# Optimization experiments

Measured on AMD Instinct MI355X. Metric: run time of the kernel, lower is better.

Reference implementation:

```python
import jax, jax.numpy as jnp
import numpy as np

N_NODES, N_EDGES, B, L = 20000, 320000, 64, 48
EMB, OUT, HEADS, HID = 256, 64, 4, 512
S_DIM, R_DIM = 64, 64
TIME_NUM, CAT_NUM = 48, 201


def lrelu(x, s=0.2):
    return jnp.where(x >= 0, x, s * x)


def gru_cell(x, h, Wi, Wh, bi, bh):
    # PyTorch GRUCell math
    gi = x @ Wi.T + bi
    gh = h @ Wh.T + bh
    ir, iz, ig = jnp.split(gi, 3, axis=-1)
    hr, hz, hg = jnp.split(gh, 3, axis=-1)
    r = jax.nn.sigmoid(ir + hr)
    z = jax.nn.sigmoid(iz + hz)
    n = jnp.tanh(ig + r * hg)
    return (1.0 - z) * n + z * h


def gru_seq(x, Wi, Wh, bi, bh, reverse=False):
    # x: [B,L,D] -> [B,L,H]
    xs = jnp.swapaxes(x, 0, 1)
    if reverse:
        xs = xs[::-1]
    h0 = jnp.zeros((x.shape[0], Wh.shape[1]), x.dtype)

    def step(h, xt):
        h2 = gru_cell(xt, h, Wi, Wh, bi, bh)
        return h2, h2

    _, ys = jax.lax.scan(step, h0, xs)
    if reverse:
        ys = ys[::-1]
    return jnp.swapaxes(ys, 0, 1)


def setup_inputs() -> dict:
    key = jax.random.key(0)
    ks = iter(jax.random.split(key, 64))
    f32 = jnp.float32

    def rn(shape, s=0.1):
        return (s * jax.random.normal(next(ks), shape)).astype(f32)

    inp = {
        'graph_x': jnp.arange(N_NODES),
        'edge_index': jax.random.randint(next(ks), (2, N_EDGES), 0, N_NODES),
        'edge_attr': jax.random.uniform(next(ks), (N_EDGES,), f32),
        'batch_x': jax.random.randint(next(ks), (B, L), 0, N_NODES),
        'batch_time': jax.random.randint(next(ks), (B, L), 0, TIME_NUM),
        'batch_cat': jax.random.randint(next(ks), (B, L), 0, CAT_NUM),
        'poi_time': jax.random.randint(next(ks), (N_NODES,), 0, TIME_NUM),
        'poi_cat': jax.random.randint(next(ks), (N_NODES,), 0, CAT_NUM),
        # params
        'node_emb': rn((N_NODES, EMB), 1.0),
        'W_gat': rn((EMB, HEADS * OUT), 0.05),
        'att_src': rn((HEADS, OUT), 0.05),
        'att_dst': rn((HEADS, OUT), 0.05),
        'gat_bias': rn((HEADS * OUT,)),
        'time_table': rn((TIME_NUM, EMB), 1.0),
        'cat_table': rn((CAT_NUM, EMB), 1.0),
        'W_w': rn((EMB, 3 * EMB)), 'b_w': rn((EMB,)),
        'Wi_f': rn((3 * HID, EMB), 0.05), 'Wh_f': rn((3 * HID, HID), 0.05),
        'bi_f': jnp.zeros((3 * HID,), f32), 'bh_f': jnp.zeros((3 * HID,), f32),
        'Wi_bw': rn((3 * HID, EMB), 0.05), 'Wh_bw': rn((3 * HID, HID), 0.05),
        'bi_bw': jnp.zeros((3 * HID,), f32), 'bh_bw': jnp.zeros((3 * HID,), f32),
        'Wi_u': rn((3 * HID, 2 * HID), 0.05), 'Wh_u': rn((3 * HID, HID), 0.05),
        'bi_u': jnp.zeros((3 * HID,), f32), 'bh_u': jnp.zeros((3 * HID,), f32),
        'Ws_m': rn((S_DIM, 2 * HID)), 'bs_m': rn((S_DIM,)),
        'Ws_lv': rn((S_DIM, 2 * HID)), 'bs_lv': rn((S_DIM,)),
        'Wr_m': rn((R_DIM, HID)), 'br_m': rn((R_DIM,)),
        'Wr_lv': rn((R_DIM, HID)), 'br_lv': rn((R_DIM,)),
        'Wp1_i': rn((3 * HID, R_DIM), 0.05), 'Wp1_h': rn((3 * HID, HID), 0.05),
        'bp1_i': jnp.zeros((3 * HID,), f32), 'bp1_h': jnp.zeros((3 * HID,), f32),
        'Wp2_i': rn((3 * HID, HID), 0.05), 'Wp2_h': rn((3 * HID, HID), 0.05),
        'bp2_i': jnp.zeros((3 * HID,), f32), 'bp2_h': jnp.zeros((3 * HID,), f32),
        'Wpm': rn((R_DIM, HID)), 'bpm': rn((R_DIM,)),
        'Wplv': rn((R_DIM, HID)), 'bplv': rn((R_DIM,)),
        'Wd': rn((N_NODES, S_DIM + R_DIM)), 'bd': rn((N_NODES,)),
    }
    return inp


def forward(graph_x, edge_index, edge_attr, batch_x, batch_time, batch_cat,
            poi_time, poi_cat, node_emb, W_gat, att_src, att_dst, gat_bias,
            time_table, cat_table, W_w, b_w, Wi_f, Wh_f, bi_f, bh_f,
            Wi_bw, Wh_bw, bi_bw, bh_bw, Wi_u, Wh_u, bi_u, bh_u,
            Ws_m, bs_m, Ws_lv, bs_lv, Wr_m, br_m, Wr_lv, br_lv,
            Wp1_i, Wp1_h, bp1_i, bp1_h, Wp2_i, Wp2_h, bp2_i, bp2_h,
            Wpm, bpm, Wplv, bplv, Wd, bd):
    Bn, Ln = batch_x.shape
    N = node_emb.shape[0]
    heads, C = att_src.shape

    # --- weighted GAT layer over the POI graph ---
    h = node_emb[graph_x]                                   # [N, EMB]
    xW = (h @ W_gat).reshape(N, heads, C)                   # [N, H, C]
    src, dst = edge_index[0], edge_index[1]
    e = lrelu((xW * att_src).sum(-1)[src] + (xW * att_dst).sum(-1)[dst])  # [E, H]
    emax = jax.ops.segment_max(e, dst, num_segments=N)
    a = jnp.exp(e - emax[dst])
    asum = jax.ops.segment_sum(a, dst, num_segments=N)
    att = a / (asum[dst] + 1e-16)
    msg = (att * edge_attr[:, None])[:, :, None] * xW[src]  # [E, H, C]
    p = jax.ops.segment_sum(msg, dst, num_segments=N).reshape(N, heads * C) + gat_bias

    # --- per-step feature build ---
    p_h = p[batch_x]                                        # [B, L, EMB]
    t_e = time_table[batch_time]
    c_e = cat_table[batch_cat]
    ph = jnp.concatenate([p_h, t_e, c_e], axis=2) @ W_w.T + b_w  # [B, L, EMB]

    # --- posterior encode: biGRU -> s, uniGRU -> r ---
    f_fwd = gru_seq(ph, Wi_f, Wh_f, bi_f, bh_f)
    f_bwd = gru_seq(ph, Wi_bw, Wh_bw, bi_bw, bh_bw, reverse=True)
    features = jnp.concatenate([f_fwd, f_bwd], axis=2)      # [B, L, 2H]
    Hh = Wh_f.shape[1]
    frontal = features[:, Ln - 1, :Hh]
    backward = features[:, 0, Hh:2 * Hh]
    g = jnp.concatenate([frontal, backward], axis=1)
    s_mean = lrelu(g @ Ws_m.T + bs_m)
    s_logvar = lrelu(g @ Ws_lv.T + bs_lv)

    key = jax.random.key(42)
    k1, k2, k3 = jax.random.split(key, 3)
    s_post = s_mean + jax.random.normal(k1, s_mean.shape, s_mean.dtype) * jnp.exp(0.5 * s_logvar)

    r_feat = gru_seq(features, Wi_u, Wh_u, bi_u, bh_u)      # [B, L, H]
    r_mean = r_feat @ Wr_m.T + br_m
    r_logvar = r_feat @ Wr_lv.T + br_lv
    r_post = r_mean + jax.random.normal(k2, r_mean.shape, r_mean.dtype) * jnp.exp(0.5 * r_logvar)

    # --- prior: 2-layer GRUCell unroll fed with shifted r_post ---
    Rd = r_post.shape[2]
    r_in = jnp.concatenate([jnp.zeros((Bn, 1, Rd), r_post.dtype), r_post[:, :-1]], axis=1)
    r_in_t = jnp.swapaxes(r_in, 0, 1)                       # [L, B, R]
    eps = jax.random.normal(k3, (Ln, Bn, Rd), r_post.dtype)

    def pstep(carry, xe):
        h1, h2 = carry
        rt, ep = xe
        h1 = gru_cell(rt, h1, Wp1_i, Wp1_h, bp1_i, bp1_h)
        h2 = gru_cell(h1, h2, Wp2_i, Wp2_h, bp2_i, bp2_h)
        mt = h2 @ Wpm.T + bpm
        lvt = h2 @ Wplv.T + bplv
        rp = mt + ep * jnp.exp(0.5 * lvt)
        return (h1, h2), (mt, lvt, rp)

    h10 = jnp.zeros((Bn, Hh), r_post.dtype)
    h20 = jnp.zeros((Bn, Hh), r_post.dtype)
    _, (ms, lvs, rps) = jax.lax.scan(pstep, (h10, h20), (r_in_t, eps))
    r_mean_prior = jnp.swapaxes(ms, 0, 1)
    r_logvar_prior = jnp.swapaxes(lvs, 0, 1)
    r_prior = jnp.swapaxes(rps, 0, 1)

    # --- decode ---
    s_expand = jnp.broadcast_to(s_post[:, None, :], (Bn, Ln, s_post.shape[1]))
    zf = jnp.concatenate([r_post, s_expand], axis=2)
    recon_x = zf @ Wd.T + bd                                # [B, L, node_num]
    return (s_mean, s_logvar, s_post, r_mean, r_logvar, r_post,
            r_mean_prior, r_logvar_prior, r_prior, recon_x)


def reference(graph_x, edge_index, edge_attr, batch_x, batch_time, batch_cat,
              poi_time, poi_cat, node_emb, W_gat, att_src, att_dst, gat_bias,
              time_table, cat_table, W_w, b_w, Wi_f, Wh_f, bi_f, bh_f,
              Wi_bw, Wh_bw, bi_bw, bh_bw, Wi_u, Wh_u, bi_u, bh_u,
              Ws_m, bs_m, Ws_lv, bs_lv, Wr_m, br_m, Wr_lv, br_lv,
              Wp1_i, Wp1_h, bp1_i, bp1_h, Wp2_i, Wp2_h, bp2_i, bp2_h,
              Wpm, bpm, Wplv, bplv, Wd, bd):
    return forward(graph_x, edge_index, edge_attr, batch_x, batch_time, batch_cat,
                   poi_time, poi_cat, node_emb, W_gat, att_src, att_dst, gat_bias,
                   time_table, cat_table, W_w, b_w, Wi_f, Wh_f, bi_f, bh_f,
                   Wi_bw, Wh_bw, bi_bw, bh_bw, Wi_u, Wh_u, bi_u, bh_u,
                   Ws_m, bs_m, Ws_lv, bs_lv, Wr_m, br_m, Wr_lv, br_lv,
                   Wp1_i, Wp1_h, bp1_i, bp1_h, Wp2_i, Wp2_h, bp2_i, bp2_h,
                   Wpm, bpm, Wplv, bplv, Wd, bd)
```

## Files before the change

kernel.cpp:

```cpp
#include <hip/hip_runtime.h>
#include <stdint.h>
#include <stddef.h>

#define DEV __device__ __forceinline__

typedef float f32x4 __attribute__((ext_vector_type(4)));
typedef short bf16x8 __attribute__((ext_vector_type(8)));

__host__ __device__ inline void tf2x32(uint32_t k0, uint32_t k1,
                                       uint32_t x0, uint32_t x1,
                                       uint32_t* o0, uint32_t* o1) {
  uint32_t ks2 = k0 ^ k1 ^ 0x1BD11BDAu;
  uint32_t ks[3] = {k0, k1, ks2};
  x0 += k0; x1 += k1;
  const uint32_t R[8] = {13u,15u,26u,6u,17u,29u,16u,24u};
  for (int r = 0; r < 5; ++r) {
    const uint32_t* rot = (r & 1) ? (R + 4) : R;
    for (int i = 0; i < 4; ++i) {
      x0 += x1;
      uint32_t d = rot[i];
      x1 = (x1 << d) | (x1 >> (32u - d));
      x1 ^= x0;
    }
    x0 += ks[(r + 1) % 3];
    x1 += ks[(r + 2) % 3] + (uint32_t)(r + 1);
  }
  *o0 = x0; *o1 = x1;
}

DEV float erfinv_approx(float x) {
  float w = -logf((1.0f - x) * (1.0f + x));
  float p;
  if (w < 5.0f) {
    w = w - 2.5f;
    p = 2.81022636e-08f;
    p = fmaf(p, w, 3.43273939e-07f);
    p = fmaf(p, w, -3.5233877e-06f);
    p = fmaf(p, w, -4.39150654e-06f);
    p = fmaf(p, w, 0.00021858087f);
    p = fmaf(p, w, -0.00125372503f);
    p = fmaf(p, w, -0.00417768164f);
    p = fmaf(p, w, 0.246640727f);
    p = fmaf(p, w, 1.50140941f);
  } else {
    w = sqrtf(w) - 3.0f;
    p = -0.000200214257f;
    p = fmaf(p, w, 0.000100950558f);
    p = fmaf(p, w, 0.00134934322f);
    p = fmaf(p, w, -0.00367342844f);
    p = fmaf(p, w, 0.00573950773f);
    p = fmaf(p, w, -0.0076224613f);
    p = fmaf(p, w, 0.00943887047f);
    p = fmaf(p, w, 1.00167406f);
    p = fmaf(p, w, 2.83297682f);
  }
  return p * x;
}

DEV float normal_part(uint32_t ka, uint32_t kb, uint32_t idx) {
  uint32_t b1, b2;
  tf2x32(ka, kb, 0u, idx, &b1, &b2);
  uint32_t bits = b1 ^ b2;
  float f = __uint_as_float((bits >> 9) | 0x3f800000u) - 1.0f;
  const float lo = -0.99999994f;
  float u = f * 2.0f + lo;
  u = fmaxf(lo, u);
  return 1.41421356f * erfinv_approx(u);
}

DEV float lrelu(float x) { return x >= 0.f ? x : 0.2f * x; }
DEV float sigm(float x) { return 1.0f / (1.0f + expf(-x)); }

DEV float gru_out(float ir, float iz, float ig, float hr, float hz, float hg, float hprev) {
  float r = sigm(ir + hr);
  float z = sigm(iz + hz);
  float n = tanhf(ig + r * hg);
  return (1.0f - z) * n + z * hprev;
}

DEV float dot4f(float4 a, float4 b, float acc) {
  return fmaf(a.x, b.x, fmaf(a.y, b.y, fmaf(a.z, b.z, fmaf(a.w, b.w, acc))));
}

template <int K4>
DEV void dot2(const float* __restrict__ h, const float* __restrict__ w0,
              const float* __restrict__ w1, float& a0, float& a1) {
  const float4* h4 = (const float4*)h;
  const float4* p0 = (const float4*)w0;
  const float4* p1 = (const float4*)w1;
  #pragma unroll 4
  for (int k = 0; k < K4; ++k) {
    float4 hv = h4[k];
    float4 v0 = p0[k], v1 = p1[k];
    a0 = dot4f(hv, v0, a0);
    a1 = dot4f(hv, v1, a1);
  }
}

template <int K4>
DEV void dotT3p(const float* __restrict__ hp, int b,
                const float* __restrict__ w0, const float* __restrict__ w1,
                const float* __restrict__ w2, float& a0, float& a1, float& a2) {
  const float4* __restrict__ w04 = (const float4*)w0;
  const float4* __restrict__ w14 = (const float4*)w1;
  const float4* __restrict__ w24 = (const float4*)w2;
  const float4* __restrict__ h4 = (const float4*)hp;
  #pragma unroll
  for (int k4 = 0; k4 < K4; ++k4) {
    float4 hv = h4[k4 * 64 + b];
    a0 = dot4f(w04[k4], hv, a0);
    a1 = dot4f(w14[k4], hv, a1);
    a2 = dot4f(w24[k4], hv, a2);
  }
}

template <int K4>
DEV void dotT3_lds(const float* __restrict__ hl, int b,
                   const float* __restrict__ w0, const float* __restrict__ w1,
                   const float* __restrict__ w2, float& a0, float& a1, float& a2) {
  const float4* __restrict__ h4 = (const float4*)hl;
  const float4* __restrict__ w04 = (const float4*)w0;
  const float4* __restrict__ w14 = (const float4*)w1;
  const float4* __restrict__ w24 = (const float4*)w2;
  #pragma unroll 8
  for (int k4 = 0; k4 < K4; ++k4) {
    float4 hv = h4[k4 * 64 + b];
    a0 = dot4f(w04[k4], hv, a0);
    a1 = dot4f(w14[k4], hv, a1);
    a2 = dot4f(w24[k4], hv, a2);
  }
}

template <int N16>
DEV void stage_lds(float* __restrict__ dst, const float* __restrict__ src) {
  const float4* __restrict__ s4 = (const float4*)src;
  float4* __restrict__ d4 = (float4*)dst;
  int tid = threadIdx.x;
  constexpr int CH = (N16 < 16) ? N16 : 16;
  #pragma unroll
  for (int r = 0; r < N16; r += CH) {
    float4 v[CH];
    #pragma unroll
    for (int u = 0; u < CH; ++u) v[u] = s4[(size_t)(r + u) * 256 + tid];
    #pragma unroll
    for (int u = 0; u < CH; ++u) d4[(size_t)(r + u) * 256 + tid] = v[u];
  }
}

DEV size_t pk(int k, int b) { return (size_t)(k >> 2) * 256 + b * 4 + (k & 3); }

DEV void coh_store_i(int* p, int v) {
  asm volatile("global_store_dword %0, %1, off sc0 sc1" :: "v"(p), "v"(v) : "memory");
}
DEV void coh_store_f(float* p, float v) {
  asm volatile("global_store_dword %0, %1, off sc0 sc1" :: "v"(p), "v"(v) : "memory");
}
DEV void coh_store_f4(float* p, f32x4 v) {
  asm volatile("global_store_dwordx4 %0, %1, off sc0 sc1" :: "v"(p), "v"(v) : "memory");
}
DEV int coh_load_i(const int* p) {
  int v;
  asm volatile("global_load_dword %0, %1, off sc0 sc1\n\ts_waitcnt vmcnt(0)"
               : "=v"(v) : "v"(p) : "memory");
  return v;
}

#define FSTRIDE 32

DEV void flag_barrier(int* __restrict__ flags, int nblk, int myidx, int gen) {
  asm volatile("s_waitcnt vmcnt(0)" ::: "memory");
  __syncthreads();
  if (threadIdx.x == 0) coh_store_i(flags + (size_t)myidx * FSTRIDE, gen);
  if ((int)threadIdx.x < nblk) {
    int spins = 0;
    while (coh_load_i(flags + (size_t)threadIdx.x * FSTRIDE) < gen) {
      __builtin_amdgcn_s_sleep(4);
      if (++spins > (1 << 21)) break;
    }
  }
  __syncthreads();
}

DEV void wait_group(const int* __restrict__ flags, int nblk, int thr) {
  if ((int)threadIdx.x < nblk) {
    int spins = 0;
    while (coh_load_i(flags + (size_t)threadIdx.x * FSTRIDE) < thr) {
      __builtin_amdgcn_s_sleep(4);
      if (++spins > (1 << 21)) break;
    }
  }
  __syncthreads();
}

DEV void store_packed_tile4(float* dst_t, const float (*smem)[64], int j0) {
  if (threadIdx.x < 64) {
    int bb = threadIdx.x;
    f32x4 v;
    v.x = smem[0][bb];
    v.y = smem[1][bb];
    v.z = smem[2][bb];
    v.w = smem[3][bb];
    coh_store_f4(dst_t + (size_t)(j0 >> 2) * 256 + bb * 4, v);
  }
}

#define GBM 128
#define GBN 128
#define GBK 16

__global__ __launch_bounds__(256) void gemm_nt(
    const float* __restrict__ A, const float* __restrict__ Bt,
    const float* __restrict__ bias, float* __restrict__ C,
    int M, int N, int K, const int* __restrict__ gatherA, int trGI) {
  __shared__ float As[GBK][GBM + 4];
  __shared__ float Bs[GBK][GBN + 4];
  const int bm = blockIdx.y * GBM;
  const int bn = blockIdx.x * GBN;
  const int tid = threadIdx.x;
  const int tx = tid & 15;
  const int ty = tid >> 4;
  float acc[8][8];
  #pragma unroll
  for (int i = 0; i < 8; ++i)
    #pragma unroll
    for (int j = 0; j < 8; ++j) acc[i][j] = 0.f;

  for (int k0 = 0; k0 < K; k0 += GBK) {
    #pragma unroll
    for (int s = 0; s < 2; ++s) {
      int f = tid + s * 256;
      int r = f >> 2, kq = f & 3;
      int row = bm + r;
      float4 v = make_float4(0.f, 0.f, 0.f, 0.f);
      if (row < M) {
        int ar = gatherA ? gatherA[row] : row;
        v = *(const float4*)&A[(size_t)ar * K + k0 + kq * 4];
      }
      As[kq * 4 + 0][r] = v.x;
      As[kq * 4 + 1][r] = v.y;
      As[kq * 4 + 2][r] = v.z;
      As[kq * 4 + 3][r] = v.w;
    }
    #pragma unroll
    for (int s = 0; s < 2; ++s) {
      int f = tid + s * 256;
      int r = f >> 2, kq = f & 3;
      int col = bn + r;
      float4 v = make_float4(0.f, 0.f, 0.f, 0.f);
      if (col < N) v = *(const float4*)&Bt[(size_t)col * K + k0 + kq * 4];
      Bs[kq * 4 + 0][r] = v.x;
      Bs[kq * 4 + 1][r] = v.y;
      Bs[kq * 4 + 2][r] = v.z;
      Bs[kq * 4 + 3][r] = v.w;
    }
    __syncthreads();
    #pragma unroll
    for (int kk = 0; kk < GBK; ++kk) {
      float4 a0 = *(const float4*)&As[kk][ty * 4];
      float4 a1 = *(const float4*)&As[kk][64 + ty * 4];
      float4 b0 = *(const float4*)&Bs[kk][tx * 4];
      float4 b1 = *(const float4*)&Bs[kk][64 + tx * 4];
      float av[8] = {a0.x, a0.y, a0.z, a0.w, a1.x, a1.y, a1.z, a1.w};
      float bv[8] = {b0.x, b0.y, b0.z, b0.w, b1.x, b1.y, b1.z, b1.w};
      #pragma unroll
      for (int i = 0; i < 8; ++i)
        #pragma unroll
        for (int j = 0; j < 8; ++j)
          acc[i][j] = fmaf(av[i], bv[j], acc[i][j]);
    }
    __syncthreads();
  }
  #pragma unroll
  for (int i = 0; i < 8; ++i) {
    int row = bm + ((i < 4) ? (ty * 4 + i) : (64 + ty * 4 + i - 4));
    if (row >= M) continue;
    if (trGI) {
      #pragma unroll
      for (int j = 0; j < 8; ++j) {
        int col = bn + ((j < 4) ? (tx * 4 + j) : (64 + tx * 4 + j - 4));
        if (col >= N) continue;
        float v = acc[i][j] + (bias ? bias[col] : 0.f);
        int bb = row / 48, tt = row - bb * 48;
        C[((size_t)tt * N + col) * 64 + bb] = v;
      }
    } else {
      #pragma unroll
      for (int g = 0; g < 2; ++g) {
        int col0 = bn + g * 64 + tx * 4;
        if (col0 + 3 >= N) continue;
        float4 v;
        v.x = acc[i][g * 4 + 0] + (bias ? bias[col0 + 0] : 0.f);
        v.y = acc[i][g * 4 + 1] + (bias ? bias[col0 + 1] : 0.f);
        v.z = acc[i][g * 4 + 2] + (bias ? bias[col0 + 2] : 0.f);
        v.w = acc[i][g * 4 + 3] + (bias ? bias[col0 + 3] : 0.f);
        *(float4*)&C[(size_t)row * N + col0] = v;
      }
    }
  }
}

__global__ void k_f32_to_bf16(const float* __restrict__ src,
                              unsigned short* __restrict__ dst, int n) {
  int i = blockIdx.x * 256 + threadIdx.x;
  if (i >= n) return;
  uint32_t u = __float_as_uint(src[i]);
  uint32_t r = (u + 0x7fffu + ((u >> 16) & 1u)) >> 16;
  dst[i] = (unsigned short)r;
}

__global__ __launch_bounds__(256) void gemm_bf16_mfma(
    const unsigned short* __restrict__ A16, const unsigned short* __restrict__ B16,
    const float* __restrict__ bias, float* __restrict__ C,
    int M, int N, int K) {
  int bm = blockIdx.x * 128;
  int bn = blockIdx.y * 128;
  int wave = threadIdx.x >> 6;
  int lane = threadIdx.x & 63;
  int wm = (wave & 1) * 64;
  int wn = (wave >> 1) * 64;
  int l15 = lane & 15;
  int kg = lane >> 4;
  f32x4 acc[4][4];
  #pragma unroll
  for (int mi = 0; mi < 4; ++mi)
    #pragma unroll
    for (int ni = 0; ni < 4; ++ni)
      acc[mi][ni] = (f32x4){0.f, 0.f, 0.f, 0.f};

  for (int kk = 0; kk < K; kk += 32) {
    bf16x8 afrag[4], bfrag[4];
    #pragma unroll
    for (int mi = 0; mi < 4; ++mi) {
      int row = bm + wm + mi * 16 + l15;
      afrag[mi] = *(const bf16x8*)&A16[(size_t)row * K + kk + kg * 8];
    }
    #pragma unroll
    for (int ni = 0; ni < 4; ++ni) {
      int col = bn + wn + ni * 16 + l15;
      if (col >= N) col = N - 1;
      bfrag[ni] = *(const bf16x8*)&B16[(size_t)col * K + kk + kg * 8];
    }
    #pragma unroll
    for (int mi = 0; mi < 4; ++mi)
      #pragma unroll
      for (int ni = 0; ni < 4; ++ni)
        acc[mi][ni] = __builtin_amdgcn_mfma_f32_16x16x32_bf16(
            afrag[mi], bfrag[ni], acc[mi][ni], 0, 0, 0);
  }
  #pragma unroll
  for (int mi = 0; mi < 4; ++mi) {
    #pragma unroll
    for (int ni = 0; ni < 4; ++ni) {
      int col = bn + wn + ni * 16 + l15;
      if (col >= N) continue;
      int rowb = bm + wm + mi * 16 + kg * 4;
      float bv = bias[col];
      #pragma unroll
      for (int r = 0; r < 4; ++r)
        C[(size_t)(rowb + r) * N + col] = acc[mi][ni][r] + bv;
    }
  }
}

__global__ void k_transpose(const float* __restrict__ W, float* __restrict__ Wt,
                            int rows, int cols) {
  int idx = blockIdx.x * 256 + threadIdx.x;
  if (idx >= rows * cols) return;
  int r = idx / cols, c = idx % cols;
  Wt[(size_t)c * rows + r] = W[idx];
}

__global__ void k_count_deg(const int* __restrict__ dst, int* __restrict__ deg, int nE) {
  int e = blockIdx.x * 256 + threadIdx.x;
  if (e < nE) atomicAdd(&deg[dst[e]], 1);
}

__global__ __launch_bounds__(1024) void k_scan(const int* __restrict__ deg,
                                               int* __restrict__ off,
                                               int* __restrict__ cursor, int n) {
  __shared__ int tmp[1024];
  __shared__ int carry_s;
  if (threadIdx.x == 0) carry_s = 0;
  __syncthreads();
  for (int base = 0; base < n; base += 1024) {
    int i = base + (int)threadIdx.x;
    int v = (i < n) ? deg[i] : 0;
    tmp[threadIdx.x] = v;
    __syncthreads();
    for (int s = 1; s < 1024; s <<= 1) {
      int t = (threadIdx.x >= (unsigned)s) ? tmp[threadIdx.x - s] : 0;
      __syncthreads();
      tmp[threadIdx.x] += t;
      __syncthreads();
    }
    int incl = tmp[threadIdx.x];
    int base_c = carry_s;
    int excl = incl - v;
    if (i < n) { off[i] = base_c + excl; cursor[i] = base_c + excl; }
    __syncthreads();
    if (threadIdx.x == 1023) carry_s = base_c + incl;
    __syncthreads();
  }
  if (threadIdx.x == 0) off[n] = carry_s;
}

__global__ void k_scatter(const int* __restrict__ dst, int* __restrict__ cursor,
                          int* __restrict__ csr, int nE) {
  int e = blockIdx.x * 256 + threadIdx.x;
  if (e < nE) {
    int pos = atomicAdd(&cursor[dst[e]], 1);
    csr[pos] = e;
  }
}

__global__ void k_alpha(const float* __restrict__ xW, const float* __restrict__ att_src,
                        const float* __restrict__ att_dst, float* __restrict__ as_,
                        float* __restrict__ ad_) {
  int i = blockIdx.x * 256 + threadIdx.x;
  if (i >= 80000) return;
  int n = i >> 2, h = i & 3;
  const float* xr = xW + (size_t)n * 256 + h * 64;
  const float* s = att_src + h * 64;
  const float* d = att_dst + h * 64;
  float a = 0.f, b = 0.f;
  dot2<16>(xr, s, d, a, b);
  as_[i] = a;
  ad_[i] = b;
}

__global__ __launch_bounds__(256) void k_gat_node(
    const float* __restrict__ xW, const float* __restrict__ as_,
    const float* __restrict__ ad_, const int* __restrict__ off,
    const int* __restrict__ csr, const int* __restrict__ esrc,
    const float* __restrict__ eattr, const float* __restrict__ gat_bias,
    float* __restrict__ p) {
  int n = blockIdx.x;
  int h = threadIdx.x >> 6;
  int c = threadIdx.x & 63;
  int s0 = off[n], s1 = off[n + 1];
  float adn = ad_[n * 4 + h];
  float m = -3.0e38f;
  for (int idx = s0; idx < s1; ++idx) {
    int e = csr[idx];
    int s = esrc[e];
    float ev = lrelu(as_[s * 4 + h] + adn);
    m = fmaxf(m, ev);
  }
  float sum = 0.f;
  for (int idx = s0; idx < s1; ++idx) {
    int e = csr[idx];
    int s = esrc[e];
    float ev = lrelu(as_[s * 4 + h] + adn);
    sum += expf(ev - m);
  }
  float acc = 0.f;
  for (int idx = s0; idx < s1; ++idx) {
    int e = csr[idx];
    int s = esrc[e];
    float ev = lrelu(as_[s * 4 + h] + adn);
    float w = expf(ev - m) / (sum + 1e-16f) * eattr[e];
    acc = fmaf(w, xW[(size_t)s * 256 + h * 64 + c], acc);
  }
  p[(size_t)n * 256 + h * 64 + c] = acc + gat_bias[h * 64 + c];
}

__global__ void k_build_X(const float* __restrict__ p, const float* __restrict__ tt,
                          const float* __restrict__ ct, const int* __restrict__ bx,
                          const int* __restrict__ btm, const int* __restrict__ bct,
                          float* __restrict__ X) {
  int idx = blockIdx.x * 256 + threadIdx.x;
  if (idx >= 3072 * 768) return;
  int rl = idx / 768, c = idx % 768;
  float v;
  if (c < 256) v = p[(size_t)bx[rl] * 256 + c];
  else if (c < 512) v = tt[(size_t)btm[rl] * 256 + (c - 256)];
  else v = ct[(size_t)bct[rl] * 256 + (c - 512)];
  X[idx] = v;
}

__global__ __launch_bounds__(256, 1) void k_gru_bidir_fused(
    const float* __restrict__ giT_f, const float* __restrict__ giT_b,
    const float* __restrict__ Wh_f, const float* __restrict__ bh_f,
    const float* __restrict__ Wh_b, const float* __restrict__ bh_b,
    float* __restrict__ features, float* __restrict__ hTb,
    int* __restrict__ flags) {
  __shared__ float lds_h[32768];
  __shared__ float smem[4][64];
  int w = threadIdx.x >> 6;
  int b = threadIdx.x & 63;
  int slot = blockIdx.x * 4 + w;
  int dir = slot >> 9;
  int j = slot & 511;
  int j0 = (blockIdx.x * 4) & 511;
  int gbid = blockIdx.x & 127;
  int* gflags = flags + (size_t)dir * 128 * FSTRIDE;
  const float* Wh = dir ? Wh_b : Wh_f;
  const float* bh = dir ? bh_b : bh_f;
  const float* gi = dir ? giT_b : giT_f;
  const float* w0 = Wh + (size_t)j * 512;
  const float* w1 = Wh + (size_t)(512 + j) * 512;
  const float* w2 = Wh + (size_t)(1024 + j) * 512;
  float bhr = bh[j], bhz = bh[512 + j], bhg = bh[1024 + j];
  float* hD = hTb + (size_t)dir * 48 * 32768;
  for (int s = 0; s < 48; ++s) {
    int t = dir ? (47 - s) : s;
    const float* gir = gi + (size_t)t * 98304;
    float giv0 = gir[j * 64 + b];
    float giv1 = gir[(512 + j) * 64 + b];
    float giv2 = gir[(1024 + j) * 64 + b];
    float hr = bhr, hz = bhz, hg = bhg, hprev = 0.f;
    if (s > 0) {
      int tp = dir ? (t + 1) : (t - 1);
      stage_lds<32>(lds_h, hD + (size_t)tp * 32768);
      __syncthreads();
      dotT3_lds<128>(lds_h, b, w0, w1, w2, hr, hz, hg);
      hprev = lds_h[pk(j, b)];
    }
    float hnew = gru_out(giv0, giv1, giv2, hr, hz, hg, hprev);
    smem[w][b] = hnew;
    features[((size_t)(b * 48 + t)) * 1024 + dir * 512 + j] = hnew;
    __syncthreads();
    store_packed_tile4(hD + (size_t)t * 32768, smem, j0);
    flag_barrier(gflags, 128, gbid, s + 1);
  }
}

__global__ __launch_bounds__(256, 1) void k_gru_u_fused(
    const float* __restrict__ giT, const float* __restrict__ Wh,
    const float* __restrict__ bh, float* __restrict__ r_feat,
    float* __restrict__ hU, int* __restrict__ flags) {
  __shared__ float lds_h[32768];
  __shared__ float smem[4][64];
  int w = threadIdx.x >> 6;
  int b = threadIdx.x & 63;
  int j = blockIdx.x * 4 + w;
  int j0 = blockIdx.x * 4;
  const float* w0 = Wh + (size_t)j * 512;
  const float* w1 = Wh + (size_t)(512 + j) * 512;
  const float* w2 = Wh + (size_t)(1024 + j) * 512;
  float bhr = bh[j], bhz = bh[512 + j], bhg = bh[1024 + j];
  for (int s = 0; s < 48; ++s) {
    const float* gir = giT + (size_t)s * 98304;
    float giv0 = gir[j * 64 + b];
    float giv1 = gir[(512 + j) * 64 + b];
    float giv2 = gir[(1024 + j) * 64 + b];
    float hr = bhr, hz = bhz, hg = bhg, hprev = 0.f;
    if (s > 0) {
      stage_lds<32>(lds_h, hU + (size_t)(s - 1) * 32768);
      __syncthreads();
      dotT3_lds<128>(lds_h, b, w0, w1, w2, hr, hz, hg);
      hprev = lds_h[pk(j, b)];
    }
    float hnew = gru_out(giv0, giv1, giv2, hr, hz, hg, hprev);
    smem[w][b] = hnew;
    r_feat[((size_t)(b * 48 + s)) * 512 + j] = hnew;
    __syncthreads();
    store_packed_tile4(hU + (size_t)s * 32768, smem, j0);
    flag_barrier(flags, 128, blockIdx.x, s + 1);
  }
}

__global__ __launch_bounds__(256, 1) void k_prior_fused(
    const float* __restrict__ r_post,
    const float* __restrict__ Wp1_i, const float* __restrict__ Wp1_h,
    const float* __restrict__ bp1_i, const float* __restrict__ bp1_h,
    const float* __restrict__ Wp2_i, const float* __restrict__ Wp2_h,
    const float* __restrict__ bp2_i, const float* __restrict__ bp2_h,
    float* __restrict__ h1S, float* __restrict__ h2S,
    float* __restrict__ rT, int* __restrict__ flags) {
  __shared__ float lds_h[32768];
  __shared__ float smem[4][64];
  int w = threadIdx.x >> 6;
  int b = threadIdx.x & 63;
  int cell = blockIdx.x >> 7;
  int gbid = blockIdx.x & 127;
  int slot = blockIdx.x * 4 + w;
  int j = slot & 511;
  int j0 = (blockIdx.x * 4) & 511;
  int* flagsA = flags;
  int* flagsB = flags + (size_t)128 * FSTRIDE;

  if (cell == 0) {
    int tid = gbid * 256 + threadIdx.x;
    for (int x = tid; x < 48 * 64 * 64; x += 32768) {
      int b0 = x & 63;
      int i0 = (x >> 6) & 63;
      int t0 = x >> 12;
      coh_store_f(rT + (size_t)t0 * 4096 + pk(i0, b0),
                  r_post[((size_t)(b0 * 48 + t0)) * 64 + i0]);
    }
    flag_barrier(flagsA, 128, gbid, 1);

    const float* wi0 = Wp1_i + (size_t)j * 64;
    const float* wi1 = Wp1_i + (size_t)(512 + j) * 64;
    const float* wi2 = Wp1_i + (size_t)(1024 + j) * 64;
    const float* wh0 = Wp1_h + (size_t)j * 512;
    const float* wh1 = Wp1_h + (size_t)(512 + j) * 512;
    const float* wh2 = Wp1_h + (size_t)(1024 + j) * 512;
    float bir = bp1_i[j], biz = bp1_i[512 + j], big = bp1_i[1024 + j];
    float bhr = bp1_h[j], bhz = bp1_h[512 + j], bhg = bp1_h[1024 + j];
    for (int k = 0; k < 48; ++k) {
      float ir = bir, iz = biz, ig = big;
      float hr = bhr, hz = bhz, hg = bhg, hprev = 0.f;
      if (k > 0) {
        stage_lds<32>(lds_h, h1S + (size_t)(k - 1) * 32768);
        dotT3p<16>(rT + (size_t)(k - 1) * 4096, b, wi0, wi1, wi2, ir, iz, ig);
        __syncthreads();
        dotT3_lds<128>(lds_h, b, wh0, wh1, wh2, hr, hz, hg);
        hprev = lds_h[pk(j, b)];
      }
      smem[w][b] = gru_out(ir, iz, ig, hr, hz, hg, hprev);
      __syncthreads();
      store_packed_tile4(h1S + (size_t)k * 32768, smem, j0);
      flag_barrier(flagsA, 128, gbid, k + 2);
    }
  } else {
    const float* wi0 = Wp2_i + (size_t)j * 512;
    const float* wi1 = Wp2_i + (size_t)(512 + j) * 512;
    const float* wi2 = Wp2_i + (size_t)(1024 + j) * 512;
    const float* wh0 = Wp2_h + (size_t)j * 512;
    const float* wh1 = Wp2_h + (size_t)(512 + j) * 512;
    const float* wh2 = Wp2_h + (size_t)(1024 + j) * 512;
    float bir = bp2_i[j], biz = bp2_i[512 + j], big = bp2_i[1024 + j];
    float bhr = bp2_h[j], bhz = bp2_h[512 + j], bhg = bp2_h[1024 + j];
    for (int t = 0; t < 48; ++t) {
      wait_group(flagsA, 128, t + 2);
      stage_lds<32>(lds_h, h1S + (size_t)t * 32768);
      __syncthreads();
      float ir = bir, iz = biz, ig = big;
      dotT3_lds<128>(lds_h, b, wi0, wi1, wi2, ir, iz, ig);
      float hr = bhr, hz = bhz, hg = bhg, hprev = 0.f;
      if (t > 0) {
        __syncthreads();
        stage_lds<32>(lds_h, h2S + (size_t)(t - 1) * 32768);
        __syncthreads();
        dotT3_lds<128>(lds_h, b, wh0, wh1, wh2, hr, hz, hg);
        hprev = lds_h[pk(j, b)];
      }
      smem[w][b] = gru_out(ir, iz, ig, hr, hz, hg, hprev);
      __syncthreads();
      store_packed_tile4(h2S + (size_t)t * 32768, smem, j0);
      flag_barrier(flagsB, 128, gbid, t + 1);
    }
  }
}

__global__ void k_s_head(const float* __restrict__ features,
                         const float* __restrict__ Ws_m, const float* __restrict__ bs_m,
                         const float* __restrict__ Ws_lv, const float* __restrict__ bs_lv,
                         float* __restrict__ out, uint32_t ka, uint32_t kb) {
  int idx = blockIdx.x * 256 + threadIdx.x;
  if (idx >= 4096) return;
  int i = idx & 63, b = idx >> 6;
  const float* fr = features + ((size_t)(b * 48 + 47)) * 1024;
  const float* bk = features + ((size_t)(b * 48 + 0)) * 1024 + 512;
  const float* wm = Ws_m + (size_t)i * 1024;
  const float* wl = Ws_lv + (size_t)i * 1024;
  float m = 0.f, lv = 0.f;
  dot2<128>(fr, wm, wl, m, lv);
  dot2<128>(bk, wm + 512, wl + 512, m, lv);
  m = lrelu(m + bs_m[i]);
  lv = lrelu(lv + bs_lv[i]);
  float nz = normal_part(ka, kb, (uint32_t)idx);
  out[idx] = m;
  out[4096 + idx] = lv;
  out[8192 + idx] = m + nz * expf(0.5f * lv);
}

__global__ void k_r_head(const float* __restrict__ r_feat,
                         const float* __restrict__ Wr_m, const float* __restrict__ br_m,
                         const float* __restrict__ Wr_lv, const float* __restrict__ br_lv,
                         float* __restrict__ out, uint32_t ka, uint32_t kb) {
  int idx = blockIdx.x * 256 + threadIdx.x;
  if (idx >= 196608) return;
  int i = idx & 63;
  int bt = idx >> 6;
  const float* f = r_feat + (size_t)bt * 512;
  float m = 0.f, lv = 0.f;
  dot2<128>(f, Wr_m + (size_t)i * 512, Wr_lv + (size_t)i * 512, m, lv);
  m += br_m[i];
  lv += br_lv[i];
  float nz = normal_part(ka, kb, (uint32_t)idx);
  out[12288 + idx] = m;
  out[208896 + idx] = lv;
  out[405504 + idx] = m + nz * expf(0.5f * lv);
}

__global__ void k_prior_out(const float* __restrict__ h2S,
                            const float* __restrict__ Wpm, const float* __restrict__ bpm,
                            const float* __restrict__ Wplv, const float* __restrict__ bplv,
                            float* __restrict__ out, uint32_t ka, uint32_t kb) {
  int idx = blockIdx.x * 256 + threadIdx.x;
  if (idx >= 196608) return;
  int i = idx & 63;
  int bt = idx >> 6;
  int b = bt & 63;
  int t = bt >> 6;
  const float4* h4 = (const float4*)(h2S + (size_t)t * 32768);
  const float4* wm4 = (const float4*)(Wpm + (size_t)i * 512);
  const float4* wl4 = (const float4*)(Wplv + (size_t)i * 512);
  float m = 0.f, lv = 0.f;
  #pragma unroll 8
  for (int k4 = 0; k4 < 128; ++k4) {
    float4 hv = h4[k4 * 64 + b];
    m = dot4f(wm4[k4], hv, m);
    lv = dot4f(wl4[k4], hv, lv);
  }
  m += bpm[i];
  lv += bplv[i];
  float ep = normal_part(ka, kb, (uint32_t)idx);
  float rp = m + ep * expf(0.5f * lv);
  size_t o = ((size_t)b * 48 + t) * 64 + i;
  out[602112 + o] = m;
  out[798720 + o] = lv;
  out[995328 + o] = rp;
}

__global__ void k_build_zf(const float* __restrict__ out, float* __restrict__ zf) {
  int idx = blockIdx.x * 256 + threadIdx.x;
  if (idx >= 3072 * 128) return;
  int row = idx >> 7, c = idx & 127;
  float v;
  if (c < 64) v = out[405504 + row * 64 + c];
  else v = out[8192 + (row / 48) * 64 + (c - 64)];
  zf[idx] = v;
}

extern "C" void kernel_launch(void* const* d_in, const int* in_sizes, int n_in,
                              void* d_out, int out_size, void* d_ws, size_t ws_size,
                              hipStream_t stream) {
  const int* graph_x = (const int*)d_in[0];
  const int* edge_index = (const int*)d_in[1];
  const float* edge_attr = (const float*)d_in[2];
  const int* batch_x = (const int*)d_in[3];
  const int* batch_time = (const int*)d_in[4];
  const int* batch_cat = (const int*)d_in[5];
  const float* node_emb = (const float*)d_in[8];
  const float* W_gat = (const float*)d_in[9];
  const float* att_src = (const float*)d_in[10];
  const float* att_dst = (const float*)d_in[11];
  const float* gat_bias = (const float*)d_in[12];
  const float* time_table = (const float*)d_in[13];
  const float* cat_table = (const float*)d_in[14];
  const float* W_w = (const float*)d_in[15];
  const float* b_w = (const float*)d_in[16];
  const float* Wi_f = (const float*)d_in[17];
  const float* Wh_f = (const float*)d_in[18];
  const float* bi_f = (const float*)d_in[19];
  const float* bh_f = (const float*)d_in[20];
  const float* Wi_bw = (const float*)d_in[21];
  const float* Wh_bw = (const float*)d_in[22];
  const float* bi_bw = (const float*)d_in[23];
  const float* bh_bw = (const float*)d_in[24];
  const float* Wi_u = (const float*)d_in[25];
  const float* Wh_u = (const float*)d_in[26];
  const float* bi_u = (const float*)d_in[27];
  const float* bh_u = (const float*)d_in[28];
  const float* Ws_m = (const float*)d_in[29];
  const float* bs_m = (const float*)d_in[30];
  const float* Ws_lv = (const float*)d_in[31];
  const float* bs_lv = (const float*)d_in[32];
  const float* Wr_m = (const float*)d_in[33];
  const float* br_m = (const float*)d_in[34];
  const float* Wr_lv = (const float*)d_in[35];
  const float* br_lv = (const float*)d_in[36];
  const float* Wp1_i = (const float*)d_in[37];
  const float* Wp1_h = (const float*)d_in[38];
  const float* bp1_i = (const float*)d_in[39];
  const float* bp1_h = (const float*)d_in[40];
  const float* Wp2_i = (const float*)d_in[41];
  const float* Wp2_h = (const float*)d_in[42];
  const float* bp2_i = (const float*)d_in[43];
  const float* bp2_h = (const float*)d_in[44];
  const float* Wpm = (const float*)d_in[45];
  const float* bpm = (const float*)d_in[46];
  const float* Wplv = (const float*)d_in[47];
  const float* bplv = (const float*)d_in[48];
  const float* Wd = (const float*)d_in[49];
  const float* bd = (const float*)d_in[50];
  float* out = (float*)d_out;

  uint32_t k1a, k1b, k2a, k2b, k3a, k3b;
  tf2x32(0u, 42u, 0u, 0u, &k1a, &k1b);
  tf2x32(0u, 42u, 0u, 1u, &k2a, &k2b);
  tf2x32(0u, 42u, 0u, 2u, &k3a, &k3b);

  float* ws = (float*)d_ws;
  size_t o = 0;
  auto alloc = [&](size_t n) { float* q = ws + o; o += n; return q; };
  float* R1 = alloc(5120000);
  float* R2 = alloc(5120000);
  float* R3 = alloc(4718592);
  float* R4 = alloc(786432);
  float* as_ = alloc(80000);
  float* ad_ = alloc(80000);
  float* Wgt = alloc(65536);
  int* deg = (int*)alloc(20000);
  int* off = (int*)alloc(20001);
  int* cursor = (int*)alloc(20000);
  int* csr = (int*)alloc(320000);
  float* rT = alloc(196608);
  int* flags = (int*)alloc(32768);

  float* xW = R1;
  float* features = R1;
  float* r_feat = R1 + 3145728;
  float* p = R2;
  float* giT_b = R2;
  float* hU = R2;
  float* X = R3;
  float* giT_f = R3;
  float* giT_u = R3;
  float* h1S = R3;
  float* h2S = R3 + 1572864;
  float* ph = R4;
  float* zf = R4;
  unsigned short* Wd16 = (unsigned short*)R2;
  unsigned short* zf16 = (unsigned short*)(R4 + 458752);
  float* hTb = out + 1191936;

  const int* esrc = edge_index;
  const int* edst = edge_index + 320000;

  dim3 B(256);

  (void)hipMemsetAsync(deg, 0, 20000 * sizeof(int), stream);
  (void)hipMemsetAsync(flags, 0, 32768 * sizeof(int), stream);

  k_transpose<<<dim3(256), B, 0, stream>>>(W_gat, Wgt, 256, 256);
  k_count_deg<<<dim3(1250), B, 0, stream>>>(edst, deg, 320000);
  k_scan<<<dim3(1), dim3(1024), 0, stream>>>(deg, off, cursor, 20000);
  k_scatter<<<dim3(1250), B, 0, stream>>>(edst, cursor, csr, 320000);
  gemm_nt<<<dim3(2, 157), B, 0, stream>>>(node_emb, Wgt, nullptr, xW,
                                          20000, 256, 256, graph_x, 0);
  k_alpha<<<dim3(313), B, 0, stream>>>(xW, att_src, att_dst, as_, ad_);
  k_gat_node<<<dim3(20000), B, 0, stream>>>(xW, as_, ad_, off, csr, esrc,
                                            edge_attr, gat_bias, p);

  k_build_X<<<dim3(9216), B, 0, stream>>>(p, time_table, cat_table, batch_x,
                                          batch_time, batch_cat, X);
  gemm_nt<<<dim3(2, 24), B, 0, stream>>>(X, W_w, b_w, ph, 3072, 256, 768,
                                         nullptr, 0);

  gemm_nt<<<dim3(12, 24), B, 0, stream>>>(ph, Wi_f, bi_f, giT_f, 3072, 1536, 256,
                                          nullptr, 1);
  gemm_nt<<<dim3(12, 24), B, 0, stream>>>(ph, Wi_bw, bi_bw, giT_b, 3072, 1536, 256,
                                          nullptr, 1);
  k_gru_bidir_fused<<<dim3(256), B, 0, stream>>>(
      giT_f, giT_b, Wh_f, bh_f, Wh_bw, bh_bw, features, hTb, flags);

  k_s_head<<<dim3(16), B, 0, stream>>>(features, Ws_m, bs_m, Ws_lv, bs_lv,
                                       out, k1a, k1b);

  gemm_nt<<<dim3(12, 24), B, 0, stream>>>(features, Wi_u, bi_u, giT_u,
                                          3072, 1536, 1024, nullptr, 1);
  k_gru_u_fused<<<dim3(128), B, 0, stream>>>(giT_u, Wh_u, bh_u, r_feat,
                                             hU, flags + 256 * FSTRIDE);

  k_f32_to_bf16<<<dim3(10000), B, 0, stream>>>(Wd, Wd16, 20000 * 128);

  k_r_head<<<dim3(768), B, 0, stream>>>(r_feat, Wr_m, br_m, Wr_lv, br_lv,
                                        out, k2a, k2b);

  k_prior_fused<<<dim3(256), B, 0, stream>>>(
      out + 405504, Wp1_i, Wp1_h, bp1_i, bp1_h, Wp2_i, Wp2_h, bp2_i, bp2_h,
      h1S, h2S, rT, flags + 384 * FSTRIDE);
  k_prior_out<<<dim3(768), B, 0, stream>>>(h2S, Wpm, bpm, Wplv, bplv,
                                           out, k3a, k3b);

  k_build_zf<<<dim3(1536), B, 0, stream>>>(out, zf);
  k_f32_to_bf16<<<dim3(1536), B, 0, stream>>>(zf, zf16, 3072 * 128);
  gemm_bf16_mfma<<<dim3(24, 157), B, 0, stream>>>(zf16, Wd16, bd,
                                                  out + 1191936, 3072, 20000, 128);
}
```

Baseline: 4.637 ms.

## Run GRU input-projection GEMMs in bf16 MFMA with a transposed store

Replaces the three fp32 gemm_nt calls that compute the GRU input gates (forward, backward and the u-GRU) with gemm_bf16_mfma. The activations and weights are first converted to bf16 in scratch buffers. A new trGI flag makes the MFMA kernel write results in the time-major, batch-innermost layout the fused GRU kernels expect. The aim is to move these matrix products onto matrix cores. In exchange it adds conversion kernels, reduces input precision to bf16, and writes scattered, strided stores.

```diff
diff --git a/kernel.cpp b/kernel.cpp
--- a/kernel.cpp
+++ b/kernel.cpp
@@ -311,7 +311,7 @@
 __global__ __launch_bounds__(256) void gemm_bf16_mfma(
     const unsigned short* __restrict__ A16, const unsigned short* __restrict__ B16,
     const float* __restrict__ bias, float* __restrict__ C,
-    int M, int N, int K) {
+    int M, int N, int K, int trGI) {
   int bm = blockIdx.x * 128;
   int bn = blockIdx.y * 128;
   int wave = threadIdx.x >> 6;
@@ -354,10 +354,19 @@
       int col = bn + wn + ni * 16 + l15;
       if (col >= N) continue;
       int rowb = bm + wm + mi * 16 + kg * 4;
-      float bv = bias[col];
-      #pragma unroll
-      for (int r = 0; r < 4; ++r)
-        C[(size_t)(rowb + r) * N + col] = acc[mi][ni][r] + bv;
+      float bv = bias ? bias[col] : 0.f;
+      if (trGI) {
+        #pragma unroll
+        for (int r = 0; r < 4; ++r) {
+          int row = rowb + r;
+          int bb = row / 48, tt = row - bb * 48;
+          C[((size_t)tt * N + col) * 64 + bb] = acc[mi][ni][r] + bv;
+        }
+      } else {
+        #pragma unroll
+        for (int r = 0; r < 4; ++r)
+          C[(size_t)(rowb + r) * N + col] = acc[mi][ni][r] + bv;
+      }
     }
   }
 }
@@ -815,6 +824,11 @@
   float* h2S = R3 + 1572864;
   float* ph = R4;
   float* zf = R4;
+  unsigned short* ph16 = (unsigned short*)R1;
+  unsigned short* Wif16 = (unsigned short*)(R1 + 1000000);
+  unsigned short* Wib16 = (unsigned short*)(R1 + 1500000);
+  unsigned short* Wiu16 = (unsigned short*)R2;
+  unsigned short* feat16 = (unsigned short*)(R2 + 1000000);
   unsigned short* Wd16 = (unsigned short*)R2;
   unsigned short* zf16 = (unsigned short*)(R4 + 458752);
   float* hTb = out + 1191936;
@@ -842,18 +856,23 @@
   gemm_nt<<<dim3(2, 24), B, 0, stream>>>(X, W_w, b_w, ph, 3072, 256, 768,
                                          nullptr, 0);
 
-  gemm_nt<<<dim3(12, 24), B, 0, stream>>>(ph, Wi_f, bi_f, giT_f, 3072, 1536, 256,
-                                          nullptr, 1);
-  gemm_nt<<<dim3(12, 24), B, 0, stream>>>(ph, Wi_bw, bi_bw, giT_b, 3072, 1536, 256,
-                                          nullptr, 1);
+  k_f32_to_bf16<<<dim3(3072), B, 0, stream>>>(ph, ph16, 3072 * 256);
+  k_f32_to_bf16<<<dim3(1536), B, 0, stream>>>(Wi_f, Wif16, 1536 * 256);
+  k_f32_to_bf16<<<dim3(1536), B, 0, stream>>>(Wi_bw, Wib16, 1536 * 256);
+  gemm_bf16_mfma<<<dim3(24, 12), B, 0, stream>>>(ph16, Wif16, bi_f, giT_f,
+                                                 3072, 1536, 256, 1);
+  gemm_bf16_mfma<<<dim3(24, 12), B, 0, stream>>>(ph16, Wib16, bi_bw, giT_b,
+                                                 3072, 1536, 256, 1);
   k_gru_bidir_fused<<<dim3(256), B, 0, stream>>>(
       giT_f, giT_b, Wh_f, bh_f, Wh_bw, bh_bw, features, hTb, flags);
 
   k_s_head<<<dim3(16), B, 0, stream>>>(features, Ws_m, bs_m, Ws_lv, bs_lv,
                                        out, k1a, k1b);
 
-  gemm_nt<<<dim3(12, 24), B, 0, stream>>>(features, Wi_u, bi_u, giT_u,
-                                          3072, 1536, 1024, nullptr, 1);
+  k_f32_to_bf16<<<dim3(12288), B, 0, stream>>>(features, feat16, 3072 * 1024);
+  k_f32_to_bf16<<<dim3(6144), B, 0, stream>>>(Wi_u, Wiu16, 1536 * 1024);
+  gemm_bf16_mfma<<<dim3(24, 12), B, 0, stream>>>(feat16, Wiu16, bi_u, giT_u,
+                                                 3072, 1536, 1024, 1);
   k_gru_u_fused<<<dim3(128), B, 0, stream>>>(giT_u, Wh_u, bh_u, r_feat,
                                              hU, flags + 256 * FSTRIDE);
 
@@ -871,5 +890,5 @@
   k_build_zf<<<dim3(1536), B, 0, stream>>>(out, zf);
   k_f32_to_bf16<<<dim3(1536), B, 0, stream>>>(zf, zf16, 3072 * 128);
   gemm_bf16_mfma<<<dim3(24, 157), B, 0, stream>>>(zf16, Wd16, bd,
-                                                  out + 1191936, 3072, 20000, 128);
-}
+                                                  out + 1191936, 3072, 20000, 128, 0);
+}
```

Measured after the change: 4.537 ms (median of 2 runs). -2.2%, faster.
